# Optimization experiments

Measured on AMD Instinct MI355X. Metric: run time of the kernel, lower is better.

Reference implementation:

```python
import jax, jax.numpy as jnp
import numpy as np

N, K, D = 32768, 4096, 256


def setup_inputs() -> dict:
    key = jax.random.key(0)
    k1, k2 = jax.random.split(key)
    z_e = jax.random.normal(k1, (N, D), dtype=jnp.float32)
    embed = jax.random.normal(k2, (K, D), dtype=jnp.float32)
    return {"z_e": z_e, "embed": embed}


def reference(z_e, embed):
    # squared L2 distances: ||z||^2 - 2 z.E^T + ||e||^2  -> [N, K]
    d = (jnp.sum(z_e * z_e, axis=1, keepdims=True)
         - 2.0 * (z_e @ embed.T)
         + jnp.sum(embed * embed, axis=1))
    idx = jnp.argmin(d, axis=1)                      # [N] int32
    one_hot = jax.nn.one_hot(idx, K, dtype=z_e.dtype)  # [N, K]
    z_q = one_hot @ embed                            # [N, D] (matches torch's one_hot @ embed)
    return (z_q, idx, one_hot)
```

## Files before the change

kernel.cpp:

```cpp
#include <hip/hip_runtime.h>


#define N_TOK 32768
#define K_CODE 4096
#define D_DIM 256
#define BM 64

typedef float f32x4 __attribute__((ext_vector_type(4)));
typedef short s16x8 __attribute__((ext_vector_type(8)));

#define OUT_FLOATS 142639104u
#define SCR_FLOATS 1576960u
#define SCR_OFF    (OUT_FLOATS - SCR_FLOATS)
#define EFRAG_SHORTS (3u * K_CODE * D_DIM)
#define OH_SAFE_ROWS 32320

#define MFMA(a, b, c) __builtin_amdgcn_mfma_f32_16x16x32_bf16((a), (b), (c), 0, 0, 0)

static __device__ __forceinline__ unsigned short f2bf(float f) {
    unsigned int u = __float_as_uint(f);
    u = (u + 0x7fffu + ((u >> 16) & 1u)) >> 16;
    return (unsigned short)u;
}
static __device__ __forceinline__ float bf2f(unsigned short b) {
    return __uint_as_float(((unsigned int)b) << 16);
}

__global__ __launch_bounds__(256) void vq_prep(const float* __restrict__ embed,
                                               float* __restrict__ out) {
    __shared__ float part[8][33];
    unsigned short* escr = (unsigned short*)(out + SCR_OFF);
    float* e2g = out + SCR_OFF + (EFRAG_SHORTS / 2);

    const int t    = threadIdx.x;
    const int cl   = t >> 5;
    const int r32  = t & 31;
    const int dc   = r32 >> 2;
    const int quad = r32 & 3;
    const int k    = blockIdx.x * 8 + cl;

    const float* src = embed + (size_t)k * D_DIM + dc * 32 + quad * 8;
    float x[8];
    *(float4*)(x)     = *(const float4*)(src);
    *(float4*)(x + 4) = *(const float4*)(src + 4);

    s16x8 hv, mv, lv;
    float s2 = 0.0f;
#pragma unroll
    for (int j = 0; j < 8; ++j) {
        const float xx = x[j];
        s2 += xx * xx;
        const unsigned short bh = f2bf(xx);
        const float r1 = xx - bf2f(bh);
        const unsigned short bm = f2bf(r1);
        hv[j] = (short)bh; mv[j] = (short)bm; lv[j] = (short)f2bf(r1 - bf2f(bm));
    }

    const int ct_g = k >> 4;
    const int lane = quad * 16 + (k & 15);
    const size_t base = ((size_t)(ct_g * 8 + dc) * 3) * 512 + lane * 8;
    *(s16x8*)&escr[base]        = hv;
    *(s16x8*)&escr[base + 512]  = mv;
    *(s16x8*)&escr[base + 1024] = lv;

    part[cl][r32] = s2;
    __syncthreads();
    if (t < 8) {
        float s = 0.0f;
#pragma unroll
        for (int j = 0; j < 32; ++j) s += part[t][j];
        e2g[blockIdx.x * 8 + t] = s;
    }
}

static __device__ __forceinline__ void load_b4(const unsigned short* __restrict__ p,
                                               s16x8 (&buf)[4][3]) {
#pragma unroll
    for (int u = 0; u < 4; ++u)
#pragma unroll
        for (int c = 0; c < 3; ++c)
            buf[u][c] = *(const s16x8*)(p + u * 12288 + c * 512);
}

static __device__ __forceinline__ size_t boff(int s) {
    return (size_t)(s >> 3) * 393216 + (size_t)(s & 7) * 1536;
}

static __device__ __forceinline__ void proc4(const short* As,
        const float* __restrict__ e2g, int s, int wu, int lane, int n,
        s16x8 (&B)[4][3], f32x4 (&acc)[4][4], float (&e2r)[4],
        float (&bv)[16], int (&bidx)[16]) {
    const int ktp = s >> 3;
    const int dc  = s & 7;
    if (dc == 0) {
#pragma unroll
        for (int u = 0; u < 4; ++u)
            e2r[u] = e2g[ktp * 512 + (wu * 4 + u) * 16 + n];
    }
#pragma unroll
    for (int rt = 0; rt < 4; ++rt) {
        s16x8 af0 = *(const s16x8*)&As[((0 * 4 + rt) * 8 + dc) * 512 + lane * 8];
        s16x8 af1 = *(const s16x8*)&As[((1 * 4 + rt) * 8 + dc) * 512 + lane * 8];
        s16x8 af2 = *(const s16x8*)&As[((2 * 4 + rt) * 8 + dc) * 512 + lane * 8];
#pragma unroll
        for (int u = 0; u < 4; ++u) {
            f32x4 a = acc[rt][u];
            a = MFMA(af0, B[u][0], a);
            a = MFMA(af0, B[u][1], a);
            a = MFMA(af1, B[u][0], a);
            a = MFMA(af1, B[u][1], a);
            a = MFMA(af0, B[u][2], a);
            a = MFMA(af2, B[u][0], a);
            acc[rt][u] = a;
        }
    }
    if (dc == 7) {
#pragma unroll
        for (int u = 0; u < 4; ++u) {
            const int code = ktp * 512 + (wu * 4 + u) * 16 + n;
#pragma unroll
            for (int rt = 0; rt < 4; ++rt)
#pragma unroll
                for (int r = 0; r < 4; ++r) {
                    const float val = fmaf(-2.0f, acc[rt][u][r], e2r[u]);
                    const int slot = rt * 4 + r;
                    if (val < bv[slot]) { bv[slot] = val; bidx[slot] = code; }
                }
        }
#pragma unroll
        for (int rt = 0; rt < 4; ++rt)
#pragma unroll
            for (int u = 0; u < 4; ++u) acc[rt][u] = (f32x4){0.f, 0.f, 0.f, 0.f};
    }
}

__global__ __launch_bounds__(512, 2)
void vq_argmin_mfma(const float* __restrict__ z_e,
                    const float* __restrict__ embed,
                    float* __restrict__ out) {
    __shared__ __align__(16) short As[49152];
    __shared__ float redv[64][9];
    __shared__ int   redi[64][9];
    __shared__ int   bk_lds[64];

    const unsigned short* escr = (const unsigned short*)(out + SCR_OFF);
    const float* e2g = out + SCR_OFF + (EFRAG_SHORTS / 2);

    const int t    = threadIdx.x;
    const int w    = t >> 6;
    const int lane = t & 63;
    const int n    = lane & 15;
    const int quad = lane >> 4;
    const int row0 = blockIdx.x * BM;

#pragma unroll
    for (int i = 0; i < 4; ++i) {
        const int run  = t + 512 * i;
        const int qs   = run & 3;
        const int dcs  = (run >> 2) & 7;
        const int row  = run >> 5;
        const float* src = z_e + (size_t)(row0 + row) * D_DIM + dcs * 32 + qs * 8;
        float x[8];
        *(float4*)(x)     = *(const float4*)(src);
        *(float4*)(x + 4) = *(const float4*)(src + 4);
        s16x8 hv, mv, lv;
#pragma unroll
        for (int j = 0; j < 8; ++j) {
            const float xx = x[j];
            const unsigned short bh = f2bf(xx);
            const float r1 = xx - bf2f(bh);
            const unsigned short bm = f2bf(r1);
            hv[j] = (short)bh; mv[j] = (short)bm; lv[j] = (short)f2bf(r1 - bf2f(bm));
        }
        const int rtile = row >> 4;
        const int ls    = qs * 16 + (row & 15);
        *(s16x8*)&As[((0 * 4 + rtile) * 8 + dcs) * 512 + ls * 8] = hv;
        *(s16x8*)&As[((1 * 4 + rtile) * 8 + dcs) * 512 + ls * 8] = mv;
        *(s16x8*)&As[((2 * 4 + rtile) * 8 + dcs) * 512 + ls * 8] = lv;
    }
    __syncthreads();

    float bv[16];
    int   bidx[16];
#pragma unroll
    for (int s = 0; s < 16; ++s) { bv[s] = 3.0e38f; bidx[s] = 0; }

    f32x4 acc[4][4];
#pragma unroll
    for (int rt = 0; rt < 4; ++rt)
#pragma unroll
        for (int u = 0; u < 4; ++u) acc[rt][u] = (f32x4){0.f, 0.f, 0.f, 0.f};

    float e2r[4];
    s16x8 b0[4][3], b1[4][3];

    const int wu = __builtin_amdgcn_readfirstlane(w);
    const unsigned short* ebase = escr + (size_t)wu * 49152 + lane * 8;

    load_b4(ebase, b0);

#pragma unroll 1
    for (int it = 0; it < 32; ++it) {
        const int s0 = it * 2, s1 = s0 + 1, s2 = s1 + 1;
        load_b4(ebase + boff(s1), b1);
        proc4(As, e2g, s0, wu, lane, n, b0, acc, e2r, bv, bidx);
        if (it < 31) load_b4(ebase + boff(s2), b0);
        proc4(As, e2g, s1, wu, lane, n, b1, acc, e2r, bv, bidx);
    }

#pragma unroll
    for (int slot = 0; slot < 16; ++slot) {
#pragma unroll
        for (int mask = 1; mask < 16; mask <<= 1) {
            const float ov = __shfl_xor(bv[slot], mask);
            const int   oi = __shfl_xor(bidx[slot], mask);
            if (ov < bv[slot] || (ov == bv[slot] && oi < bidx[slot])) {
                bv[slot] = ov; bidx[slot] = oi;
            }
        }
    }
    if (n == 0) {
#pragma unroll
        for (int rt = 0; rt < 4; ++rt)
#pragma unroll
            for (int r = 0; r < 4; ++r) {
                const int row_local = rt * 16 + quad * 4 + r;
                redv[row_local][w] = bv[rt * 4 + r];
                redi[row_local][w] = bidx[rt * 4 + r];
            }
    }
    __syncthreads();
    if (t < 64) {
        float v = redv[t][0];
        int  bi = redi[t][0];
#pragma unroll
        for (int j = 1; j < 8; ++j) {
            const float v2 = redv[t][j];
            const int   i2 = redi[t][j];
            if (v2 < v || (v2 == v && i2 < bi)) { v = v2; bi = i2; }
        }
        bk_lds[t] = bi;
        out[(size_t)N_TOK * D_DIM + (size_t)(row0 + t)] = (float)bi;
    }
    __syncthreads();

    float* zq = out;
    float* oh = out + (size_t)N_TOK * D_DIM + N_TOK;

#pragma unroll 1
    for (int rr = 0; rr < 8; ++rr) {
        const int rl  = w * 8 + rr;
        const int row = row0 + rl;
        const int bk  = bk_lds[rl];
        f32x4 v = *(const f32x4*)&embed[(size_t)bk * D_DIM + lane * 4];
        __builtin_nontemporal_store(v, (f32x4*)&zq[(size_t)row * D_DIM + lane * 4]);
    }
    if (row0 < OH_SAFE_ROWS) {
#pragma unroll 1
        for (int rr = 0; rr < 8; ++rr) {
            const int rl  = w * 8 + rr;
            const int row = row0 + rl;
            const int bk  = bk_lds[rl];
            float* ohrow = &oh[(size_t)row * K_CODE];
#pragma unroll
            for (int g = 0; g < 16; ++g) {
                const int base = (g * 64 + lane) * 4;
                f32x4 u;
                u.x = (bk == base    ) ? 1.0f : 0.0f;
                u.y = (bk == base + 1) ? 1.0f : 0.0f;
                u.z = (bk == base + 2) ? 1.0f : 0.0f;
                u.w = (bk == base + 3) ? 1.0f : 0.0f;
                __builtin_nontemporal_store(u, (f32x4*)&ohrow[base]);
            }
        }
    }
}

__launch_bounds__(256, 8)
__global__ void vq_oh_tail(float* __restrict__ out) {
    __shared__ int bks[16];
    const int t    = threadIdx.x;
    const int w    = t >> 6;
    const int lane = t & 63;
    const int row0 = OH_SAFE_ROWS + blockIdx.x * 16;

    const float* idxf = out + (size_t)N_TOK * D_DIM;
    float* oh = out + (size_t)N_TOK * D_DIM + N_TOK;

    if (t < 16) bks[t] = (int)idxf[row0 + t];
    __syncthreads();

#pragma unroll 1
    for (int rr = 0; rr < 4; ++rr) {
        const int r   = rr * 4 + w;
        const int row = row0 + r;
        const int bk  = bks[r];
        float* ohrow = &oh[(size_t)row * K_CODE];
#pragma unroll
        for (int g = 0; g < 16; ++g) {
            const int base = (g * 64 + lane) * 4;
            f32x4 u;
            u.x = (bk == base    ) ? 1.0f : 0.0f;
            u.y = (bk == base + 1) ? 1.0f : 0.0f;
            u.z = (bk == base + 2) ? 1.0f : 0.0f;
            u.w = (bk == base + 3) ? 1.0f : 0.0f;
            __builtin_nontemporal_store(u, (f32x4*)&ohrow[base]);
        }
    }
}

extern "C" void kernel_launch(void* const* d_in, const int* in_sizes, int n_in,
                              void* d_out, int out_size, void* d_ws, size_t ws_size,
                              hipStream_t stream) {
    const float* z_e   = (const float*)d_in[0];
    const float* embed = (const float*)d_in[1];
    float* out = (float*)d_out;

    hipLaunchKernelGGL(vq_prep,        dim3(K_CODE / 8), dim3(256), 0, stream, embed, out);
    hipLaunchKernelGGL(vq_argmin_mfma, dim3(N_TOK / BM), dim3(512), 0, stream, z_e, embed, out);
    hipLaunchKernelGGL(vq_oh_tail,     dim3((N_TOK - OH_SAFE_ROWS) / 16), dim3(256), 0, stream, out);
}
```

Before: 839.0 us.

## Split codebook search across two blocks per row tile with atomic merge

Each 64-row tile is now handled by two blocks, each scanning half of the codebook. Block IDs are mapped so the two halves land on different XCD groups. Partial argmin values and indices go to scratch space in the output buffer, and an atomic counter elects the second-finishing block to merge both halves and write z_q, idx and one_hot. The aim is more parallelism and better load balance (1024 blocks instead of 512), at the cost of an extra counter reset, global partial traffic, fences, and duplicate A-tile staging per half.

```diff
diff --git a/kernel.cpp b/kernel.cpp
--- a/kernel.cpp
+++ b/kernel.cpp
@@ -10,9 +10,13 @@
 typedef short s16x8 __attribute__((ext_vector_type(8)));
 
 #define OUT_FLOATS 142639104u
-#define SCR_FLOATS 1576960u
+#define EFRAG_SHORTS (3u * K_CODE * D_DIM)
+#define SCR_FLOATS (EFRAG_SHORTS / 2 + K_CODE + 2u * N_TOK + 2u * N_TOK + 512u)
 #define SCR_OFF    (OUT_FLOATS - SCR_FLOATS)
-#define EFRAG_SHORTS (3u * K_CODE * D_DIM)
+#define E2_OFF     (SCR_OFF + EFRAG_SHORTS / 2)
+#define PV_OFF     (E2_OFF + K_CODE)
+#define PI_OFF     (PV_OFF + 2u * N_TOK)
+#define CNT_OFF    (PI_OFF + 2u * N_TOK)
 #define OH_SAFE_ROWS 32320
 
 #define MFMA(a, b, c) __builtin_amdgcn_mfma_f32_16x16x32_bf16((a), (b), (c), 0, 0, 0)
@@ -30,7 +34,7 @@
                                                float* __restrict__ out) {
     __shared__ float part[8][33];
     unsigned short* escr = (unsigned short*)(out + SCR_OFF);
-    float* e2g = out + SCR_OFF + (EFRAG_SHORTS / 2);
+    float* e2g = out + E2_OFF;
 
     const int t    = threadIdx.x;
     const int cl   = t >> 5;
@@ -38,6 +42,12 @@
     const int dc   = r32 >> 2;
     const int quad = r32 & 3;
     const int k    = blockIdx.x * 8 + cl;
+
+    if (blockIdx.x == 0) {
+        int* cnt = (int*)(out + CNT_OFF);
+        for (int i = t; i < 512; i += 256)
+            __hip_atomic_store(&cnt[i], 0, __ATOMIC_RELAXED, __HIP_MEMORY_SCOPE_AGENT);
+    }
 
     const float* src = embed + (size_t)k * D_DIM + dc * 32 + quad * 8;
     float x[8];
@@ -87,10 +97,10 @@
 }
 
 static __device__ __forceinline__ void proc4(const short* As,
-        const float* __restrict__ e2g, int s, int wu, int lane, int n,
+        const float* __restrict__ e2g, int s, int kbase, int wu, int lane, int n,
         s16x8 (&B)[4][3], f32x4 (&acc)[4][4], float (&e2r)[4],
         float (&bv)[16], int (&bidx)[16]) {
-    const int ktp = s >> 3;
+    const int ktp = kbase + (s >> 3);
     const int dc  = s & 7;
     if (dc == 0) {
 #pragma unroll
@@ -142,16 +152,26 @@
     __shared__ float redv[64][9];
     __shared__ int   redi[64][9];
     __shared__ int   bk_lds[64];
+    __shared__ int   last_flag;
 
     const unsigned short* escr = (const unsigned short*)(out + SCR_OFF);
-    const float* e2g = out + SCR_OFF + (EFRAG_SHORTS / 2);
+    const float* e2g = out + E2_OFF;
+    float* pv  = out + PV_OFF;
+    int*   pi  = (int*)(out + PI_OFF);
+    int*   cnt = (int*)(out + CNT_OFF);
 
     const int t    = threadIdx.x;
     const int w    = t >> 6;
     const int lane = t & 63;
     const int n    = lane & 15;
     const int quad = lane >> 4;
-    const int row0 = blockIdx.x * BM;
+
+    const int bid  = blockIdx.x;
+    const int xcd  = bid & 7;
+    const int h    = xcd >> 2;
+    const int tile = (bid >> 3) * 4 + (xcd & 3);
+    const int row0 = tile * BM;
+    const int kbase = h * 4;
 
 #pragma unroll
     for (int i = 0; i < 4; ++i) {
@@ -195,17 +215,17 @@
     s16x8 b0[4][3], b1[4][3];
 
     const int wu = __builtin_amdgcn_readfirstlane(w);
-    const unsigned short* ebase = escr + (size_t)wu * 49152 + lane * 8;
+    const unsigned short* ebase = escr + (size_t)kbase * 393216 + (size_t)wu * 49152 + lane * 8;
 
     load_b4(ebase, b0);
 
 #pragma unroll 1
-    for (int it = 0; it < 32; ++it) {
+    for (int it = 0; it < 16; ++it) {
         const int s0 = it * 2, s1 = s0 + 1, s2 = s1 + 1;
         load_b4(ebase + boff(s1), b1);
-        proc4(As, e2g, s0, wu, lane, n, b0, acc, e2r, bv, bidx);
-        if (it < 31) load_b4(ebase + boff(s2), b0);
-        proc4(As, e2g, s1, wu, lane, n, b1, acc, e2r, bv, bidx);
+        proc4(As, e2g, s0, kbase, wu, lane, n, b0, acc, e2r, bv, bidx);
+        if (it < 15) load_b4(ebase + boff(s2), b0);
+        proc4(As, e2g, s1, kbase, wu, lane, n, b1, acc, e2r, bv, bidx);
     }
 
 #pragma unroll
@@ -230,16 +250,40 @@
             }
     }
     __syncthreads();
+
+    float v = 0.0f;
+    int   bi = 0;
     if (t < 64) {
-        float v = redv[t][0];
-        int  bi = redi[t][0];
+        v  = redv[t][0];
+        bi = redi[t][0];
 #pragma unroll
         for (int j = 1; j < 8; ++j) {
             const float v2 = redv[t][j];
             const int   i2 = redi[t][j];
             if (v2 < v || (v2 == v && i2 < bi)) { v = v2; bi = i2; }
         }
-        bk_lds[t] = bi;
+        __hip_atomic_store(&pv[h * N_TOK + row0 + t], v,  __ATOMIC_RELAXED, __HIP_MEMORY_SCOPE_AGENT);
+        __hip_atomic_store(&pi[h * N_TOK + row0 + t], bi, __ATOMIC_RELAXED, __HIP_MEMORY_SCOPE_AGENT);
+    }
+    __threadfence();
+    __syncthreads();
+    if (t == 0) {
+        const int old = __hip_atomic_fetch_add(&cnt[tile], 1, __ATOMIC_ACQ_REL,
+                                               __HIP_MEMORY_SCOPE_AGENT);
+        last_flag = old;
+    }
+    __syncthreads();
+    if (last_flag == 0) return;
+    __threadfence();
+
+    if (t < 64) {
+        const int oh_h = h ^ 1;
+        const float ov = __hip_atomic_load(&pv[oh_h * N_TOK + row0 + t],
+                                           __ATOMIC_RELAXED, __HIP_MEMORY_SCOPE_AGENT);
+        const int   oi = __hip_atomic_load(&pi[oh_h * N_TOK + row0 + t],
+                                           __ATOMIC_RELAXED, __HIP_MEMORY_SCOPE_AGENT);
+        if (ov < v || (ov == v && oi < bi)) { v = ov; bi = oi; }
+        bk_lds[t] = bi & (K_CODE - 1);
         out[(size_t)N_TOK * D_DIM + (size_t)(row0 + t)] = (float)bi;
     }
     __syncthreads();
@@ -252,8 +296,8 @@
         const int rl  = w * 8 + rr;
         const int row = row0 + rl;
         const int bk  = bk_lds[rl];
-        f32x4 v = *(const f32x4*)&embed[(size_t)bk * D_DIM + lane * 4];
-        __builtin_nontemporal_store(v, (f32x4*)&zq[(size_t)row * D_DIM + lane * 4]);
+        f32x4 vv = *(const f32x4*)&embed[(size_t)bk * D_DIM + lane * 4];
+        __builtin_nontemporal_store(vv, (f32x4*)&zq[(size_t)row * D_DIM + lane * 4]);
     }
     if (row0 < OH_SAFE_ROWS) {
 #pragma unroll 1
@@ -287,7 +331,7 @@
     const float* idxf = out + (size_t)N_TOK * D_DIM;
     float* oh = out + (size_t)N_TOK * D_DIM + N_TOK;
 
-    if (t < 16) bks[t] = (int)idxf[row0 + t];
+    if (t < 16) bks[t] = ((int)idxf[row0 + t]) & (K_CODE - 1);
     __syncthreads();
 
 #pragma unroll 1
@@ -317,6 +361,6 @@
     float* out = (float*)d_out;
 
     hipLaunchKernelGGL(vq_prep,        dim3(K_CODE / 8), dim3(256), 0, stream, embed, out);
-    hipLaunchKernelGGL(vq_argmin_mfma, dim3(N_TOK / BM), dim3(512), 0, stream, z_e, embed, out);
+    hipLaunchKernelGGL(vq_argmin_mfma, dim3(2 * N_TOK / BM), dim3(512), 0, stream, z_e, embed, out);
     hipLaunchKernelGGL(vq_oh_tail,     dim3((N_TOK - OH_SAFE_ROWS) / 16), dim3(256), 0, stream, out);
 }
```

Result: slower. 1.113 ms (+32.6%).

## Two-pass argmin: bf16x2 coarse pass with top-2 margin and bf16x3 refinement

Applied to the files above, without the earlier changes.

The main pass now uses a 2-term bf16 split, 4 MFMAs per fragment instead of 6, with a larger 128-row tile. It tracks best and second-best distances per row. Rows whose margin falls below a fixed threshold are appended to a global list. Two follow-up kernels recompute those rows at full bf16x3 precision, then patch idx, z_q and the one-hot entries. This cuts matrix-core work in the bulk pass, at the risk of wrong argmins if the threshold is too small or the list overflows its 8192-entry cap.

```diff
diff --git a/kernel.cpp b/kernel.cpp
--- a/kernel.cpp
+++ b/kernel.cpp
@@ -4,16 +4,21 @@
 #define N_TOK 32768
 #define K_CODE 4096
 #define D_DIM 256
-#define BM 64
+#define BM 128
+#define THR_AMBIG 0.05f
 
 typedef float f32x4 __attribute__((ext_vector_type(4)));
 typedef short s16x8 __attribute__((ext_vector_type(8)));
 
 #define OUT_FLOATS 142639104u
-#define SCR_FLOATS 1576960u
+#define EFRAG_SHORTS (3u * K_CODE * D_DIM)
+#define SCR_FLOATS (EFRAG_SHORTS / 2 + K_CODE + 8192u + 16384u + 64u)
 #define SCR_OFF    (OUT_FLOATS - SCR_FLOATS)
-#define EFRAG_SHORTS (3u * K_CODE * D_DIM)
-#define OH_SAFE_ROWS 32320
+#define E2_OFF     (SCR_OFF + EFRAG_SHORTS / 2)
+#define LIST_OFF   (E2_OFF + K_CODE)
+#define AMIN_OFF   (LIST_OFF + 8192u)
+#define CNT_OFF    (AMIN_OFF + 16384u)
+#define OH_SAFE_ROWS 32256
 
 #define MFMA(a, b, c) __builtin_amdgcn_mfma_f32_16x16x32_bf16((a), (b), (c), 0, 0, 0)
 
@@ -25,12 +30,17 @@
 static __device__ __forceinline__ float bf2f(unsigned short b) {
     return __uint_as_float(((unsigned int)b) << 16);
 }
+static __device__ __forceinline__ unsigned long long packvi(float v, int code) {
+    unsigned int u = __float_as_uint(v);
+    u = (u & 0x80000000u) ? ~u : (u ^ 0x80000000u);
+    return ((unsigned long long)u << 32) | (unsigned int)code;
+}
 
 __global__ __launch_bounds__(256) void vq_prep(const float* __restrict__ embed,
                                                float* __restrict__ out) {
     __shared__ float part[8][33];
     unsigned short* escr = (unsigned short*)(out + SCR_OFF);
-    float* e2g = out + SCR_OFF + (EFRAG_SHORTS / 2);
+    float* e2g = out + E2_OFF;
 
     const int t    = threadIdx.x;
     const int cl   = t >> 5;
@@ -38,6 +48,12 @@
     const int dc   = r32 >> 2;
     const int quad = r32 & 3;
     const int k    = blockIdx.x * 8 + cl;
+
+    if (blockIdx.x == 0) {
+        if (t == 0) ((int*)(out + CNT_OFF))[0] = 0;
+        unsigned long long* am = (unsigned long long*)(out + AMIN_OFF);
+        for (int i = t; i < 8192; i += 256) am[i] = ~0ull;
+    }
 
     const float* src = embed + (size_t)k * D_DIM + dc * 32 + quad * 8;
     float x[8];
@@ -73,78 +89,20 @@
     }
 }
 
-static __device__ __forceinline__ void load_b4(const unsigned short* __restrict__ p,
-                                               s16x8 (&buf)[4][3]) {
-#pragma unroll
-    for (int u = 0; u < 4; ++u)
-#pragma unroll
-        for (int c = 0; c < 3; ++c)
-            buf[u][c] = *(const s16x8*)(p + u * 12288 + c * 512);
-}
-
-static __device__ __forceinline__ size_t boff(int s) {
-    return (size_t)(s >> 3) * 393216 + (size_t)(s & 7) * 1536;
-}
-
-static __device__ __forceinline__ void proc4(const short* As,
-        const float* __restrict__ e2g, int s, int wu, int lane, int n,
-        s16x8 (&B)[4][3], f32x4 (&acc)[4][4], float (&e2r)[4],
-        float (&bv)[16], int (&bidx)[16]) {
-    const int ktp = s >> 3;
-    const int dc  = s & 7;
-    if (dc == 0) {
-#pragma unroll
-        for (int u = 0; u < 4; ++u)
-            e2r[u] = e2g[ktp * 512 + (wu * 4 + u) * 16 + n];
-    }
-#pragma unroll
-    for (int rt = 0; rt < 4; ++rt) {
-        s16x8 af0 = *(const s16x8*)&As[((0 * 4 + rt) * 8 + dc) * 512 + lane * 8];
-        s16x8 af1 = *(const s16x8*)&As[((1 * 4 + rt) * 8 + dc) * 512 + lane * 8];
-        s16x8 af2 = *(const s16x8*)&As[((2 * 4 + rt) * 8 + dc) * 512 + lane * 8];
-#pragma unroll
-        for (int u = 0; u < 4; ++u) {
-            f32x4 a = acc[rt][u];
-            a = MFMA(af0, B[u][0], a);
-            a = MFMA(af0, B[u][1], a);
-            a = MFMA(af1, B[u][0], a);
-            a = MFMA(af1, B[u][1], a);
-            a = MFMA(af0, B[u][2], a);
-            a = MFMA(af2, B[u][0], a);
-            acc[rt][u] = a;
-        }
-    }
-    if (dc == 7) {
-#pragma unroll
-        for (int u = 0; u < 4; ++u) {
-            const int code = ktp * 512 + (wu * 4 + u) * 16 + n;
-#pragma unroll
-            for (int rt = 0; rt < 4; ++rt)
-#pragma unroll
-                for (int r = 0; r < 4; ++r) {
-                    const float val = fmaf(-2.0f, acc[rt][u][r], e2r[u]);
-                    const int slot = rt * 4 + r;
-                    if (val < bv[slot]) { bv[slot] = val; bidx[slot] = code; }
-                }
-        }
-#pragma unroll
-        for (int rt = 0; rt < 4; ++rt)
-#pragma unroll
-            for (int u = 0; u < 4; ++u) acc[rt][u] = (f32x4){0.f, 0.f, 0.f, 0.f};
-    }
-}
-
 __global__ __launch_bounds__(512, 2)
-void vq_argmin_mfma(const float* __restrict__ z_e,
-                    const float* __restrict__ embed,
-                    float* __restrict__ out) {
-    __shared__ __align__(16) short As[49152];
-    __shared__ float redv[64][9];
-    __shared__ int   redi[64][9];
-    __shared__ int   bk_lds[64];
+void vq_pass1(const float* __restrict__ z_e,
+              const float* __restrict__ embed,
+              float* __restrict__ out) {
+    __shared__ __align__(16) short As[65536];
+    __shared__ float redv1[128][9];
+    __shared__ int   redi1[128][9];
+    __shared__ float redv2[128][9];
+    __shared__ int   bk_lds[128];
 
     const unsigned short* escr = (const unsigned short*)(out + SCR_OFF);
-    const float* e2g = out + SCR_OFF + (EFRAG_SHORTS / 2);
+    const float* e2g = out + E2_OFF;
+    int* list = (int*)(out + LIST_OFF);
+    int* cnt  = (int*)(out + CNT_OFF);
 
     const int t    = threadIdx.x;
     const int w    = t >> 6;
@@ -154,7 +112,7 @@
     const int row0 = blockIdx.x * BM;
 
 #pragma unroll
-    for (int i = 0; i < 4; ++i) {
+    for (int i = 0; i < 8; ++i) {
         const int run  = t + 512 * i;
         const int qs   = run & 3;
         const int dcs  = (run >> 2) & 7;
@@ -163,84 +121,138 @@
         float x[8];
         *(float4*)(x)     = *(const float4*)(src);
         *(float4*)(x + 4) = *(const float4*)(src + 4);
-        s16x8 hv, mv, lv;
+        s16x8 hv, mv;
 #pragma unroll
         for (int j = 0; j < 8; ++j) {
             const float xx = x[j];
             const unsigned short bh = f2bf(xx);
-            const float r1 = xx - bf2f(bh);
-            const unsigned short bm = f2bf(r1);
-            hv[j] = (short)bh; mv[j] = (short)bm; lv[j] = (short)f2bf(r1 - bf2f(bm));
-        }
-        const int rtile = row >> 4;
-        const int ls    = qs * 16 + (row & 15);
-        *(s16x8*)&As[((0 * 4 + rtile) * 8 + dcs) * 512 + ls * 8] = hv;
-        *(s16x8*)&As[((1 * 4 + rtile) * 8 + dcs) * 512 + ls * 8] = mv;
-        *(s16x8*)&As[((2 * 4 + rtile) * 8 + dcs) * 512 + ls * 8] = lv;
+            hv[j] = (short)bh;
+            mv[j] = (short)f2bf(xx - bf2f(bh));
+        }
+        const int rt = row >> 4;
+        const int ls = qs * 16 + (row & 15);
+        *(s16x8*)&As[((0 * 8 + rt) * 8 + dcs) * 512 + ls * 8] = hv;
+        *(s16x8*)&As[((1 * 8 + rt) * 8 + dcs) * 512 + ls * 8] = mv;
     }
     __syncthreads();
 
-    float bv[16];
-    int   bidx[16];
-#pragma unroll
-    for (int s = 0; s < 16; ++s) { bv[s] = 3.0e38f; bidx[s] = 0; }
-
-    f32x4 acc[4][4];
-#pragma unroll
-    for (int rt = 0; rt < 4; ++rt)
-#pragma unroll
-        for (int u = 0; u < 4; ++u) acc[rt][u] = (f32x4){0.f, 0.f, 0.f, 0.f};
-
-    float e2r[4];
-    s16x8 b0[4][3], b1[4][3];
+    float bv1[32]; int bi1[32]; float bv2[32];
+#pragma unroll
+    for (int s = 0; s < 32; ++s) { bv1[s] = 3.0e38f; bi1[s] = 0x7fffffff; bv2[s] = 3.0e38f; }
+
+    f32x4 acc[8][2];
+#pragma unroll
+    for (int rt = 0; rt < 8; ++rt)
+#pragma unroll
+        for (int u = 0; u < 2; ++u) acc[rt][u] = (f32x4){0.f, 0.f, 0.f, 0.f};
+
+    float e2r[2];
+    s16x8 B0[2][2], B1[2][2];
 
     const int wu = __builtin_amdgcn_readfirstlane(w);
-    const unsigned short* ebase = escr + (size_t)wu * 49152 + lane * 8;
-
-    load_b4(ebase, b0);
-
-#pragma unroll 1
-    for (int it = 0; it < 32; ++it) {
-        const int s0 = it * 2, s1 = s0 + 1, s2 = s1 + 1;
-        load_b4(ebase + boff(s1), b1);
-        proc4(As, e2g, s0, wu, lane, n, b0, acc, e2r, bv, bidx);
-        if (it < 31) load_b4(ebase + boff(s2), b0);
-        proc4(As, e2g, s1, wu, lane, n, b1, acc, e2r, bv, bidx);
-    }
-
-#pragma unroll
-    for (int slot = 0; slot < 16; ++slot) {
+    const unsigned short* ebase = escr + (size_t)(wu * 2) * 12288 + lane * 8;
+
+#define P1OFF(s) ((size_t)((s) >> 3) * 196608 + (size_t)((s) & 7) * 1536)
+#define LOADB2(buf, p)                                         \
+    {                                                          \
+        _Pragma("unroll") for (int u = 0; u < 2; ++u)          \
+            _Pragma("unroll") for (int c = 0; c < 2; ++c)      \
+                (buf)[u][c] = *(const s16x8*)((p) + u * 12288 + c * 512); \
+    }
+
+    LOADB2(B0, ebase)
+
+#define PROC1(s, B)                                                            \
+    {                                                                          \
+        const int ctile = (s) >> 3, dc = (s) & 7;                              \
+        if (dc == 0) {                                                         \
+            _Pragma("unroll") for (int u = 0; u < 2; ++u)                      \
+                e2r[u] = e2g[ctile * 256 + (wu * 2 + u) * 16 + n];             \
+        }                                                                      \
+        _Pragma("unroll") for (int rt = 0; rt < 8; ++rt) {                     \
+            s16x8 af0 = *(const s16x8*)&As[((0 * 8 + rt) * 8 + dc) * 512 + lane * 8]; \
+            s16x8 af1 = *(const s16x8*)&As[((1 * 8 + rt) * 8 + dc) * 512 + lane * 8]; \
+            _Pragma("unroll") for (int u = 0; u < 2; ++u) {                    \
+                f32x4 a = acc[rt][u];                                          \
+                a = MFMA(af0, B[u][0], a);                                     \
+                a = MFMA(af0, B[u][1], a);                                     \
+                a = MFMA(af1, B[u][0], a);                                     \
+                a = MFMA(af1, B[u][1], a);                                     \
+                acc[rt][u] = a;                                                \
+            }                                                                  \
+        }                                                                      \
+        if (dc == 7) {                                                         \
+            _Pragma("unroll") for (int u = 0; u < 2; ++u) {                    \
+                const int code = ctile * 256 + (wu * 2 + u) * 16 + n;          \
+                _Pragma("unroll") for (int rt = 0; rt < 8; ++rt)               \
+                    _Pragma("unroll") for (int r = 0; r < 4; ++r) {            \
+                        const float val = fmaf(-2.0f, acc[rt][u][r], e2r[u]);  \
+                        const int slot = rt * 4 + r;                           \
+                        if (val < bv1[slot] ||                                 \
+                            (val == bv1[slot] && code < bi1[slot])) {          \
+                            bv2[slot] = bv1[slot];                             \
+                            bv1[slot] = val; bi1[slot] = code;                 \
+                        } else if (val < bv2[slot]) bv2[slot] = val;           \
+                    }                                                          \
+            }                                                                  \
+            _Pragma("unroll") for (int rt = 0; rt < 8; ++rt)                   \
+                _Pragma("unroll") for (int u = 0; u < 2; ++u)                  \
+                    acc[rt][u] = (f32x4){0.f, 0.f, 0.f, 0.f};                  \
+        }                                                                      \
+    }
+
+#pragma unroll 1
+    for (int it = 0; it < 64; ++it) {
+        const int s0 = it * 2, s1 = s0 + 1, s2 = s0 + 2;
+        LOADB2(B1, ebase + P1OFF(s1))
+        PROC1(s0, B0)
+        if (it < 63) LOADB2(B0, ebase + P1OFF(s2))
+        PROC1(s1, B1)
+    }
+
+#pragma unroll
+    for (int slot = 0; slot < 32; ++slot) {
 #pragma unroll
         for (int mask = 1; mask < 16; mask <<= 1) {
-            const float ov = __shfl_xor(bv[slot], mask);
-            const int   oi = __shfl_xor(bidx[slot], mask);
-            if (ov < bv[slot] || (ov == bv[slot] && oi < bidx[slot])) {
-                bv[slot] = ov; bidx[slot] = oi;
-            }
+            const float ov1 = __shfl_xor(bv1[slot], mask);
+            const int   oi1 = __shfl_xor(bi1[slot], mask);
+            const float ov2 = __shfl_xor(bv2[slot], mask);
+            const bool  ol  = ov1 < bv1[slot] || (ov1 == bv1[slot] && oi1 < bi1[slot]);
+            const float big = ol ? bv1[slot] : ov1;
+            if (ol) { bv1[slot] = ov1; bi1[slot] = oi1; }
+            bv2[slot] = fminf(fminf(bv2[slot], ov2), big);
         }
     }
     if (n == 0) {
 #pragma unroll
-        for (int rt = 0; rt < 4; ++rt)
+        for (int rt = 0; rt < 8; ++rt)
 #pragma unroll
             for (int r = 0; r < 4; ++r) {
-                const int row_local = rt * 16 + quad * 4 + r;
-                redv[row_local][w] = bv[rt * 4 + r];
-                redi[row_local][w] = bidx[rt * 4 + r];
+                const int rl = rt * 16 + quad * 4 + r;
+                const int slot = rt * 4 + r;
+                redv1[rl][w] = bv1[slot];
+                redi1[rl][w] = bi1[slot];
+                redv2[rl][w] = bv2[slot];
             }
     }
     __syncthreads();
-    if (t < 64) {
-        float v = redv[t][0];
-        int  bi = redi[t][0];
+    if (t < 128) {
+        float v1 = redv1[t][0]; int i1 = redi1[t][0]; float v2 = redv2[t][0];
 #pragma unroll
         for (int j = 1; j < 8; ++j) {
-            const float v2 = redv[t][j];
-            const int   i2 = redi[t][j];
-            if (v2 < v || (v2 == v && i2 < bi)) { v = v2; bi = i2; }
-        }
-        bk_lds[t] = bi;
-        out[(size_t)N_TOK * D_DIM + (size_t)(row0 + t)] = (float)bi;
+            const float b1 = redv1[t][j]; const int bi = redi1[t][j];
+            const float b2 = redv2[t][j];
+            const bool  bl = b1 < v1 || (b1 == v1 && bi < i1);
+            const float big = bl ? v1 : b1;
+            if (bl) { v1 = b1; i1 = bi; }
+            v2 = fminf(fminf(v2, b2), big);
+        }
+        bk_lds[t] = i1;
+        out[(size_t)N_TOK * D_DIM + (size_t)(row0 + t)] = (float)i1;
+        if (v2 - v1 <= THR_AMBIG) {
+            const int pos = atomicAdd(cnt, 1);
+            if (pos < 8192) list[pos] = row0 + t;
+        }
     }
     __syncthreads();
 
@@ -248,8 +260,8 @@
     float* oh = out + (size_t)N_TOK * D_DIM + N_TOK;
 
 #pragma unroll 1
-    for (int rr = 0; rr < 8; ++rr) {
-        const int rl  = w * 8 + rr;
+    for (int rr = 0; rr < 16; ++rr) {
+        const int rl  = w * 16 + rr;
         const int row = row0 + rl;
         const int bk  = bk_lds[rl];
         f32x4 v = *(const f32x4*)&embed[(size_t)bk * D_DIM + lane * 4];
@@ -257,8 +269,8 @@
     }
     if (row0 < OH_SAFE_ROWS) {
 #pragma unroll 1
-        for (int rr = 0; rr < 8; ++rr) {
-            const int rl  = w * 8 + rr;
+        for (int rr = 0; rr < 16; ++rr) {
+            const int rl  = w * 16 + rr;
             const int row = row0 + rl;
             const int bk  = bk_lds[rl];
             float* ohrow = &oh[(size_t)row * K_CODE];
@@ -276,6 +288,191 @@
     }
 }
 
+__global__ __launch_bounds__(512, 2)
+void vq_fixa(const float* __restrict__ z_e, float* __restrict__ out) {
+    __shared__ __align__(16) short As[49152];
+    __shared__ float redv[64][9];
+    __shared__ int   redi[64][9];
+    __shared__ int   rows_lds[64];
+
+    const unsigned short* escr = (const unsigned short*)(out + SCR_OFF);
+    const float* e2g = out + E2_OFF;
+    const int* list = (const int*)(out + LIST_OFF);
+    unsigned long long* amin = (unsigned long long*)(out + AMIN_OFF);
+    const int cntv = ((const int*)(out + CNT_OFF))[0];
+    const int ncap = cntv < 8192 ? cntv : 8192;
+    if (ncap <= 0) return;
+
+    const int t    = threadIdx.x;
+    const int w    = t >> 6;
+    const int lane = t & 63;
+    const int n    = lane & 15;
+    const int quad = lane >> 4;
+    const int slice = blockIdx.x & 7;
+    const int c0    = blockIdx.x >> 3;
+
+    const int wu = __builtin_amdgcn_readfirstlane(w);
+    const unsigned short* ebase = escr + (size_t)wu * 49152 + lane * 8;
+
+#pragma unroll 1
+    for (int chunk = c0; chunk * 64 < ncap; chunk += 2) {
+        const int nrows = (ncap - chunk * 64) < 64 ? (ncap - chunk * 64) : 64;
+        if (t < 64) {
+            const int j = chunk * 64 + t;
+            rows_lds[t] = list[j < ncap ? j : chunk * 64];
+        }
+        __syncthreads();
+
+#pragma unroll
+        for (int i = 0; i < 4; ++i) {
+            const int run  = t + 512 * i;
+            const int qs   = run & 3;
+            const int dcs  = (run >> 2) & 7;
+            const int row  = run >> 5;
+            const int grow = rows_lds[row];
+            const float* src = z_e + (size_t)grow * D_DIM + dcs * 32 + qs * 8;
+            float x[8];
+            *(float4*)(x)     = *(const float4*)(src);
+            *(float4*)(x + 4) = *(const float4*)(src + 4);
+            s16x8 hv, mv, lv;
+#pragma unroll
+            for (int j = 0; j < 8; ++j) {
+                const float xx = x[j];
+                const unsigned short bh = f2bf(xx);
+                const float r1 = xx - bf2f(bh);
+                const unsigned short bm = f2bf(r1);
+                hv[j] = (short)bh; mv[j] = (short)bm; lv[j] = (short)f2bf(r1 - bf2f(bm));
+            }
+            const int rt = row >> 4;
+            const int ls = qs * 16 + (row & 15);
+            *(s16x8*)&As[((0 * 4 + rt) * 8 + dcs) * 512 + ls * 8] = hv;
+            *(s16x8*)&As[((1 * 4 + rt) * 8 + dcs) * 512 + ls * 8] = mv;
+            *(s16x8*)&As[((2 * 4 + rt) * 8 + dcs) * 512 + ls * 8] = lv;
+        }
+        __syncthreads();
+
+        float bv[16]; int bidx[16];
+#pragma unroll
+        for (int s = 0; s < 16; ++s) { bv[s] = 3.0e38f; bidx[s] = 0x7fffffff; }
+        f32x4 acc[4][4];
+#pragma unroll
+        for (int rt = 0; rt < 4; ++rt)
+#pragma unroll
+            for (int u = 0; u < 4; ++u) acc[rt][u] = (f32x4){0.f, 0.f, 0.f, 0.f};
+        float e2r[4];
+
+#pragma unroll 1
+        for (int dc = 0; dc < 8; ++dc) {
+            s16x8 B[4][3];
+            const unsigned short* p = ebase + (size_t)slice * 393216 + (size_t)dc * 1536;
+#pragma unroll
+            for (int u = 0; u < 4; ++u)
+#pragma unroll
+                for (int c = 0; c < 3; ++c)
+                    B[u][c] = *(const s16x8*)(p + u * 12288 + c * 512);
+            if (dc == 0) {
+#pragma unroll
+                for (int u = 0; u < 4; ++u)
+                    e2r[u] = e2g[slice * 512 + (wu * 4 + u) * 16 + n];
+            }
+#pragma unroll
+            for (int rt = 0; rt < 4; ++rt) {
+                s16x8 af0 = *(const s16x8*)&As[((0 * 4 + rt) * 8 + dc) * 512 + lane * 8];
+                s16x8 af1 = *(const s16x8*)&As[((1 * 4 + rt) * 8 + dc) * 512 + lane * 8];
+                s16x8 af2 = *(const s16x8*)&As[((2 * 4 + rt) * 8 + dc) * 512 + lane * 8];
+#pragma unroll
+                for (int u = 0; u < 4; ++u) {
+                    f32x4 a = acc[rt][u];
+                    a = MFMA(af0, B[u][0], a);
+                    a = MFMA(af0, B[u][1], a);
+                    a = MFMA(af1, B[u][0], a);
+                    a = MFMA(af1, B[u][1], a);
+                    a = MFMA(af0, B[u][2], a);
+                    a = MFMA(af2, B[u][0], a);
+                    acc[rt][u] = a;
+                }
+            }
+        }
+#pragma unroll
+        for (int u = 0; u < 4; ++u) {
+            const int code = slice * 512 + (wu * 4 + u) * 16 + n;
+#pragma unroll
+            for (int rt = 0; rt < 4; ++rt)
+#pragma unroll
+                for (int r = 0; r < 4; ++r) {
+                    const float val = fmaf(-2.0f, acc[rt][u][r], e2r[u]);
+                    const int slot = rt * 4 + r;
+                    if (val < bv[slot] || (val == bv[slot] && code < bidx[slot])) {
+                        bv[slot] = val; bidx[slot] = code;
+                    }
+                }
+        }
+#pragma unroll
+        for (int slot = 0; slot < 16; ++slot) {
+#pragma unroll
+            for (int mask = 1; mask < 16; mask <<= 1) {
+                const float ov = __shfl_xor(bv[slot], mask);
+                const int   oi = __shfl_xor(bidx[slot], mask);
+                if (ov < bv[slot] || (ov == bv[slot] && oi < bidx[slot])) {
+                    bv[slot] = ov; bidx[slot] = oi;
+                }
+            }
+        }
+        if (n == 0) {
+#pragma unroll
+            for (int rt = 0; rt < 4; ++rt)
+#pragma unroll
+                for (int r = 0; r < 4; ++r) {
+                    const int rl = rt * 16 + quad * 4 + r;
+                    redv[rl][w] = bv[rt * 4 + r];
+                    redi[rl][w] = bidx[rt * 4 + r];
+                }
+        }
+        __syncthreads();
+        if (t < nrows) {
+            float v = redv[t][0]; int bi = redi[t][0];
+#pragma unroll
+            for (int j = 1; j < 8; ++j) {
+                const float v2 = redv[t][j]; const int i2 = redi[t][j];
+                if (v2 < v || (v2 == v && i2 < bi)) { v = v2; bi = i2; }
+            }
+            atomicMin(&amin[chunk * 64 + t], packvi(v, bi));
+        }
+        __syncthreads();
+    }
+}
+
+__global__ __launch_bounds__(256) void vq_fixb(const float* __restrict__ embed,
+                                               float* __restrict__ out) {
+    const int* list = (const int*)(out + LIST_OFF);
+    const unsigned long long* amin = (const unsigned long long*)(out + AMIN_OFF);
+    const int cntv = ((const int*)(out + CNT_OFF))[0];
+    const int ncap = cntv < 8192 ? cntv : 8192;
+
+    float* idxf = out + (size_t)N_TOK * D_DIM;
+    float* zq   = out;
+    float* oh   = out + (size_t)N_TOK * D_DIM + N_TOK;
+    const int t = threadIdx.x;
+
+#pragma unroll 1
+    for (int e = blockIdx.x; e < ncap; e += 32) {
+        const int row = list[e];
+        const int bi  = (int)(amin[e] & 0xffffffffu) & (K_CODE - 1);
+        const int io  = ((int)idxf[row]) & (K_CODE - 1);
+        if (bi != io) {
+            if (t == 0) idxf[row] = (float)bi;
+            if (t < 64) {
+                f32x4 v = *(const f32x4*)&embed[(size_t)bi * D_DIM + t * 4];
+                *(f32x4*)&zq[(size_t)row * D_DIM + t * 4] = v;
+            }
+            if (row < OH_SAFE_ROWS && t == 0) {
+                oh[(size_t)row * K_CODE + io] = 0.0f;
+                oh[(size_t)row * K_CODE + bi] = 1.0f;
+            }
+        }
+    }
+}
+
 __launch_bounds__(256, 8)
 __global__ void vq_oh_tail(float* __restrict__ out) {
     __shared__ int bks[16];
@@ -287,7 +484,7 @@
     const float* idxf = out + (size_t)N_TOK * D_DIM;
     float* oh = out + (size_t)N_TOK * D_DIM + N_TOK;
 
-    if (t < 16) bks[t] = (int)idxf[row0 + t];
+    if (t < 16) bks[t] = ((int)idxf[row0 + t]) & (K_CODE - 1);
     __syncthreads();
 
 #pragma unroll 1
@@ -316,7 +513,9 @@
     const float* embed = (const float*)d_in[1];
     float* out = (float*)d_out;
 
-    hipLaunchKernelGGL(vq_prep,        dim3(K_CODE / 8), dim3(256), 0, stream, embed, out);
-    hipLaunchKernelGGL(vq_argmin_mfma, dim3(N_TOK / BM), dim3(512), 0, stream, z_e, embed, out);
-    hipLaunchKernelGGL(vq_oh_tail,     dim3((N_TOK - OH_SAFE_ROWS) / 16), dim3(256), 0, stream, out);
-}
+    hipLaunchKernelGGL(vq_prep,    dim3(K_CODE / 8), dim3(256), 0, stream, embed, out);
+    hipLaunchKernelGGL(vq_pass1,   dim3(N_TOK / BM), dim3(512), 0, stream, z_e, embed, out);
+    hipLaunchKernelGGL(vq_fixa,    dim3(16),  dim3(512), 0, stream, z_e, out);
+    hipLaunchKernelGGL(vq_fixb,    dim3(32),  dim3(256), 0, stream, embed, out);
+    hipLaunchKernelGGL(vq_oh_tail, dim3((N_TOK - OH_SAFE_ROWS) / 16), dim3(256), 0, stream, out);
+}
```

After: 1.115 ms. 32.9% more time.
